# Kernel tuning notes

Measured on AMD Instinct MI355X. Metric: run time of the kernel, lower is better.

The kernel has to match this reference:

```python
import jax, jax.numpy as jnp
import numpy as np
from jax import lax

B, C_IN, C_OUT, H, W, E = 16, 256, 256, 32, 32, 8


def setup_inputs() -> dict:
    key = jax.random.key(0)
    k = jax.random.split(key, 5)
    x = jax.random.normal(k[0], (B, C_IN, H, W), dtype=jnp.float32)
    # router: Conv2d(C_IN, E, kernel_size=1) -> weight [E, C_IN], bias [E]
    wc = jax.random.normal(k[1], (E, C_IN), dtype=jnp.float32) / np.sqrt(C_IN)
    bc = jnp.zeros((E,), dtype=jnp.float32)
    # experts: E x Conv2d(C_IN, C_OUT, 3, padding=1) + ReLU
    we = jax.random.normal(k[2], (E, C_OUT, C_IN, 3, 3), dtype=jnp.float32) / np.sqrt(C_IN * 9)
    be = jnp.zeros((E, C_OUT), dtype=jnp.float32)
    return {"x": x, "wc": wc, "bc": bc, "we": we, "be": be}


def reference(x, wc, bc, we, be):
    Bx = x.shape[0]
    # controller: 1x1 conv then global avg-pool == pool then linear
    pooled = jnp.mean(x, axis=(2, 3))                      # [B, C_IN]
    logits = pooled @ wc.T + bc                            # [B, E]
    decisions = jnp.argmax(logits, axis=1)                 # [B] int
    # run ALL experts on the full batch as one grouped conv: weight [E*C_OUT, C_IN, 3, 3]
    w_all = we.reshape(E * C_OUT, C_IN, 3, 3)
    y = lax.conv_general_dilated(
        x, w_all, window_strides=(1, 1), padding="SAME",
        dimension_numbers=("NCHW", "OIHW", "NCHW"))        # [B, E*C_OUT, H, W]
    y = y + be.reshape(1, E * C_OUT, 1, 1)
    y = jax.nn.relu(y).reshape(Bx, E, C_OUT, H, W)
    # faithful to forward_test: out block i is components[dec[i]](x) for the FULL batch
    # out[i*B + j] = y[j, dec[i]]
    gathered = y[:, decisions]                             # [j, i, C_OUT, H, W]
    out = jnp.swapaxes(gathered, 0, 1).reshape(Bx * Bx, C_OUT, H, W)
    return out
```

## Files before the change

kernel.cpp:

```cpp
#include <hip/hip_runtime.h>
#include <hip/hip_bf16.h>
#include <stdint.h>

#define B_    16
#define CIN   256
#define COUT  256
#define E_    8
#define HW    1024
#define PH    34
#define PW    34

typedef __attribute__((ext_vector_type(8))) short  short8;
typedef __attribute__((ext_vector_type(4))) float  floatx4;

#define XT_OFF 17408
#define XT_BYTES (B_*PH*PW*CIN*2)
#define WT_OFF (XT_OFF + XT_BYTES)

__device__ __forceinline__ void gld_lds16(const void* g, void* l) {
    __builtin_amdgcn_global_load_lds(
        (const __attribute__((address_space(1))) unsigned int*)g,
        (__attribute__((address_space(3))) unsigned int*)l,
        16, 0, 0);
}

__global__ void prep_kernel(const float* __restrict__ x, const float* __restrict__ we,
                            unsigned short* __restrict__ xt, unsigned short* __restrict__ wt,
                            float* __restrict__ pooled) {
    int bid = blockIdx.x;
    int t = threadIdx.x;
    if (bid < 128) {
        int b = bid >> 3, ci0 = (bid & 7) * 32;
        __shared__ float tileF[32][65];
        float psum[8];
        #pragma unroll
        for (int li = 0; li < 8; ++li) psum[li] = 0.0f;
        int hwl = t & 63, wv = t >> 6;
        int hwl2 = t >> 2, grp = t & 3;
        for (int chunk = 0; chunk < 16; ++chunk) {
            #pragma unroll
            for (int li = 0; li < 8; ++li) {
                int ci = wv + li*4;
                float v = x[((size_t)b*CIN + ci0 + ci)*HW + chunk*64 + hwl];
                tileF[ci][hwl] = v;
                psum[li] += v;
            }
            __syncthreads();
            int hw = chunk*64 + hwl2;
            int h = hw >> 5, w = hw & 31;
            short8 v8;
            #pragma unroll
            for (int q = 0; q < 8; ++q) {
                __hip_bfloat16 hv = __float2bfloat16(tileF[grp*8 + q][hwl2]);
                v8[q] = *(short*)&hv;
            }
            *(short8*)&xt[(((size_t)b*PH + h + 1)*PW + (w + 1))*CIN + ci0 + grp*8] = v8;
            __syncthreads();
        }
        #pragma unroll
        for (int li = 0; li < 8; ++li) {
            float s = psum[li];
            #pragma unroll
            for (int o = 32; o > 0; o >>= 1) s += __shfl_down(s, o, 64);
            if ((t & 63) == 0) pooled[b*CIN + ci0 + wv + li*4] = s;
        }
        short8 z = {0,0,0,0,0,0,0,0};
        for (int idx = t; idx < 528; idx += 256) {
            int pos = idx >> 2, sub = idx & 3;
            int h, w;
            if (pos < 34)       { h = 0;            w = pos; }
            else if (pos < 68)  { h = 33;           w = pos - 34; }
            else if (pos < 100) { h = pos - 68 + 1; w = 0; }
            else                { h = pos - 100 + 1;w = 33; }
            *(short8*)&xt[(((size_t)b*PH + h)*PW + w)*CIN + ci0 + sub*8] = z;
        }
    } else {
        int wbid = bid - 128;
        int e = wbid >> 8, co = wbid & 255;
        __shared__ float buf[CIN*9];
        const float* src = we + ((size_t)e*COUT + co)*CIN*9;
        #pragma unroll
        for (int k = 0; k < 9; ++k) buf[t + k*256] = src[t + k*256];
        __syncthreads();
        for (int idx = t; idx < 288; idx += 256) {
            int rs = idx >> 5, grp = idx & 31;
            short8 v;
            #pragma unroll
            for (int q = 0; q < 8; ++q) {
                __hip_bfloat16 h = __float2bfloat16(buf[(grp*8 + q)*9 + rs]);
                v[q] = *(short*)&h;
            }
            *(short8*)&wt[(((size_t)e*9 + rs)*COUT + co)*CIN + grp*8] = v;
        }
    }
}

__global__ __launch_bounds__(256) void conv_kernel(
    const unsigned short* __restrict__ xt, const unsigned short* __restrict__ wt,
    const float* __restrict__ pooled, const float* __restrict__ wc,
    const float* __restrict__ bc, const float* __restrict__ be,
    float* __restrict__ out) {

    int tile = blockIdx.x;
    int b = blockIdx.y;
    int e = blockIdx.z;
    int mt = tile >> 3, nt = tile & 7;
    int t = threadIdx.x;

    __shared__ float lg[16][8];
    __shared__ int sdec[16];
    if (t < 128) {
        int bb = t >> 3, ee = t & 7;
        float acc = 0.0f;
        const float4* pp = (const float4*)(pooled + bb*CIN);
        const float4* ww = (const float4*)(wc + ee*CIN);
        #pragma unroll 4
        for (int i = 0; i < CIN/4; ++i) {
            float4 p = pp[i], w = ww[i];
            acc += p.x*w.x + p.y*w.y + p.z*w.z + p.w*w.w;
        }
        lg[bb][ee] = acc * (1.0f/1024.0f) + bc[ee];
    }
    __syncthreads();
    if (t < 16) {
        float best = lg[t][0]; int bi = 0;
        #pragma unroll
        for (int j = 1; j < 8; ++j) if (lg[t][j] > best) { best = lg[t][j]; bi = j; }
        sdec[t] = bi;
    }
    __syncthreads();
    int dcs[16];
    #pragma unroll
    for (int i = 0; i < 16; ++i) dcs[i] = sdec[i];
    bool active = false;
    #pragma unroll
    for (int i = 0; i < 16; ++i) active |= (dcs[i] == e);
    if (!active) return;

    __shared__ __align__(16) unsigned short sA[2][512*8];
    __shared__ __align__(16) unsigned short sB[2][1024*8];

    int wave = t >> 6, lane = t & 63;
    int wm = wave >> 1, wn = wave & 1;
    int kg = lane >> 4, ln = lane & 15;

    int ph0 = nt * 4;
    int co0 = mt * 128;

    floatx4 acc[4][4];
    #pragma unroll
    for (int i = 0; i < 4; ++i)
        #pragma unroll
        for (int j = 0; j < 4; ++j) acc[i][j] = (floatx4)0.0f;

    const unsigned short* xb = xt + ((size_t)b*PH + ph0)*PW*CIN;
    const unsigned short* wb = wt + (size_t)e*9*COUT*CIN + (size_t)co0*CIN;

    auto stageA = [&](int ck, int sh, int buf) {
        const unsigned short* wsrc = wb + (size_t)sh*COUT*CIN + ck*32;
        #pragma unroll
        for (int k = 0; k < 2; ++k) {
            int c = t + k*256;
            int row = c >> 2, gs = c & 3;
            int g = gs ^ ((row >> 1) & 3);
            gld_lds16(wsrc + (size_t)row*CIN + g*8, &sA[buf][c*8]);
        }
    };
    auto stageB = [&](int ck, int buf) {
        const unsigned short* xsrc = xb + ck*32;
        #pragma unroll
        for (int k = 0; k < 3; ++k) {
            int c = t + k*256;
            int rB = c >> 2, gs = c & 3;
            int g = gs ^ ((rB >> 1) & 3);
            gld_lds16(xsrc + (size_t)rB*CIN + g*8, &sB[buf][c*8]);
        }
        if (t < 64) {
            int c = t + 768;
            int cc = c < 816 ? c : 815;
            int rB = cc >> 2, gs = cc & 3;
            int g = gs ^ ((rB >> 1) & 3);
            gld_lds16(xsrc + (size_t)rB*CIN + g*8, &sB[buf][c*8]);
        }
    };

    stageB(0, 0);
    stageA(0, 0, 0);
    __syncthreads();

    for (int ck = 0; ck < 8; ++ck) {
        for (int sh = 0; sh < 9; ++sh) {
            int it = ck*9 + sh;
            int ab = it & 1, bb_ = ck & 1;

            if (sh < 8) {
                stageA(ck, sh + 1, ab ^ 1);
            } else if (ck < 7) {
                stageA(ck + 1, 0, ab ^ 1);
                stageB(ck + 1, bb_ ^ 1);
            }

            short8 a[4], bv[4];
            #pragma unroll
            for (int im = 0; im < 4; ++im) {
                int row = wm*64 + im*16 + ln;
                int cL = row*4 + (kg ^ ((row >> 1) & 3));
                a[im] = *(const short8*)(&sA[ab][cL*8]);
            }
            int r = sh / 3, s = sh - r*3;
            #pragma unroll
            for (int in = 0; in < 4; ++in) {
                int n  = wn*64 + in*16 + ln;
                int hl = n >> 5, wl = n & 31;
                int rB = (hl + r)*34 + (wl + s);
                int cL = rB*4 + (kg ^ ((rB >> 1) & 3));
                bv[in] = *(const short8*)(&sB[bb_][cL*8]);
            }

            #pragma unroll
            for (int im = 0; im < 4; ++im)
                #pragma unroll
                for (int in = 0; in < 4; ++in)
                    acc[im][in] = __builtin_amdgcn_mfma_f32_16x16x32_bf16(bv[in], a[im], acc[im][in], 0, 0, 0);

            __syncthreads();
        }
    }

    float bias[4];
    #pragma unroll
    for (int im = 0; im < 4; ++im)
        bias[im] = be[e*COUT + co0 + wm*64 + im*16 + ln];
    #pragma unroll
    for (int im = 0; im < 4; ++im)
        #pragma unroll
        for (int in = 0; in < 4; ++in)
            #pragma unroll
            for (int rg = 0; rg < 4; ++rg) {
                float v = acc[im][in][rg] + bias[im];
                acc[im][in][rg] = v > 0.0f ? v : 0.0f;
            }

    for (int i = 0; i < 16; ++i) {
        if (dcs[i] != e) continue;
        float* ob = out + (size_t)(i*16 + b)*COUT*HW;
        #pragma unroll
        for (int im = 0; im < 4; ++im) {
            int co = co0 + wm*64 + im*16 + ln;
            float* orow = ob + (size_t)co*HW + nt*128 + wn*64 + kg*4;
            #pragma unroll
            for (int in = 0; in < 4; ++in)
                *(floatx4*)(orow + in*16) = acc[im][in];
        }
    }
}

extern "C" void kernel_launch(void* const* d_in, const int* in_sizes, int n_in,
                              void* d_out, int out_size, void* d_ws, size_t ws_size,
                              hipStream_t stream) {
    const float* x  = (const float*)d_in[0];
    const float* wc = (const float*)d_in[1];
    const float* bc = (const float*)d_in[2];
    const float* we = (const float*)d_in[3];
    const float* be = (const float*)d_in[4];
    float* out = (float*)d_out;

    char* ws = (char*)d_ws;
    float* pooled = (float*)(ws + 64);
    unsigned short* xt = (unsigned short*)(ws + XT_OFF);
    unsigned short* wt = (unsigned short*)(ws + WT_OFF);

    prep_kernel<<<2176, 256, 0, stream>>>(x, we, xt, wt, pooled);
    conv_kernel<<<dim3(16, 16, 8), 256, 0, stream>>>(xt, wt, pooled, wc, bc, be, out);
}
```

Before: 481.4 us.

## Move routing to separate kernel and single-buffer the input tile in LDS

Routing logits and argmax now run once in a small decide_kernel instead of being recomputed by every conv block. The conv kernel drops the double buffer for the input patch, cutting LDS use per block, which may allow more resident blocks. The patch reload is now done only at each channel-chunk boundary, behind an explicit barrier after the last shift's B reads. The cost is less overlap of the B load with compute and one extra kernel launch.

```diff
diff --git a/kernel.cpp b/kernel.cpp
--- a/kernel.cpp
+++ b/kernel.cpp
@@ -95,51 +95,52 @@
     }
 }
 
-__global__ __launch_bounds__(256) void conv_kernel(
+__global__ void decide_kernel(const float* __restrict__ pooled, const float* __restrict__ wc,
+                              const float* __restrict__ bc, int* __restrict__ dec) {
+    int t = threadIdx.x;
+    int b = t >> 3, e = t & 7;
+    float acc = 0.0f;
+    const float4* pp = (const float4*)(pooled + b*CIN);
+    const float4* ww = (const float4*)(wc + e*CIN);
+    #pragma unroll 4
+    for (int i = 0; i < CIN/4; ++i) {
+        float4 p = pp[i], w = ww[i];
+        acc += p.x*w.x + p.y*w.y + p.z*w.z + p.w*w.w;
+    }
+    acc = acc * (1.0f/1024.0f) + bc[e];
+    __shared__ float lg[16][8];
+    lg[b][e] = acc;
+    __syncthreads();
+    if (e == 0) {
+        float best = lg[b][0]; int bi = 0;
+        #pragma unroll
+        for (int j = 1; j < 8; ++j) { if (lg[b][j] > best) { best = lg[b][j]; bi = j; } }
+        dec[b] = bi;
+    }
+}
+
+__global__ void conv_kernel(
     const unsigned short* __restrict__ xt, const unsigned short* __restrict__ wt,
-    const float* __restrict__ pooled, const float* __restrict__ wc,
-    const float* __restrict__ bc, const float* __restrict__ be,
+    const float* __restrict__ be, const int* __restrict__ dec,
     float* __restrict__ out) {
 
     int tile = blockIdx.x;
     int b = blockIdx.y;
     int e = blockIdx.z;
     int mt = tile >> 3, nt = tile & 7;
-    int t = threadIdx.x;
-
-    __shared__ float lg[16][8];
-    __shared__ int sdec[16];
-    if (t < 128) {
-        int bb = t >> 3, ee = t & 7;
-        float acc = 0.0f;
-        const float4* pp = (const float4*)(pooled + bb*CIN);
-        const float4* ww = (const float4*)(wc + ee*CIN);
-        #pragma unroll 4
-        for (int i = 0; i < CIN/4; ++i) {
-            float4 p = pp[i], w = ww[i];
-            acc += p.x*w.x + p.y*w.y + p.z*w.z + p.w*w.w;
-        }
-        lg[bb][ee] = acc * (1.0f/1024.0f) + bc[ee];
-    }
-    __syncthreads();
-    if (t < 16) {
-        float best = lg[t][0]; int bi = 0;
-        #pragma unroll
-        for (int j = 1; j < 8; ++j) if (lg[t][j] > best) { best = lg[t][j]; bi = j; }
-        sdec[t] = bi;
-    }
-    __syncthreads();
+
     int dcs[16];
     #pragma unroll
-    for (int i = 0; i < 16; ++i) dcs[i] = sdec[i];
+    for (int i = 0; i < 16; ++i) dcs[i] = dec[i];
     bool active = false;
     #pragma unroll
     for (int i = 0; i < 16; ++i) active |= (dcs[i] == e);
     if (!active) return;
 
     __shared__ __align__(16) unsigned short sA[2][512*8];
-    __shared__ __align__(16) unsigned short sB[2][1024*8];
-
+    __shared__ __align__(16) unsigned short sB[832*8];
+
+    int t = threadIdx.x;
     int wave = t >> 6, lane = t & 63;
     int wm = wave >> 1, wn = wave & 1;
     int kg = lane >> 4, ln = lane & 15;
@@ -166,64 +167,80 @@
             gld_lds16(wsrc + (size_t)row*CIN + g*8, &sA[buf][c*8]);
         }
     };
-    auto stageB = [&](int ck, int buf) {
+    auto stageB = [&](int ck) {
         const unsigned short* xsrc = xb + ck*32;
         #pragma unroll
         for (int k = 0; k < 3; ++k) {
             int c = t + k*256;
             int rB = c >> 2, gs = c & 3;
             int g = gs ^ ((rB >> 1) & 3);
-            gld_lds16(xsrc + (size_t)rB*CIN + g*8, &sB[buf][c*8]);
+            gld_lds16(xsrc + (size_t)rB*CIN + g*8, &sB[c*8]);
         }
         if (t < 64) {
             int c = t + 768;
             int cc = c < 816 ? c : 815;
             int rB = cc >> 2, gs = cc & 3;
             int g = gs ^ ((rB >> 1) & 3);
-            gld_lds16(xsrc + (size_t)rB*CIN + g*8, &sB[buf][c*8]);
-        }
-    };
-
-    stageB(0, 0);
+            gld_lds16(xsrc + (size_t)rB*CIN + g*8, &sB[c*8]);
+        }
+    };
+
+    short8 a[4], bv[4];
+    auto readA = [&](int ab) {
+        #pragma unroll
+        for (int im = 0; im < 4; ++im) {
+            int row = wm*64 + im*16 + ln;
+            int cL = row*4 + (kg ^ ((row >> 1) & 3));
+            a[im] = *(const short8*)(&sA[ab][cL*8]);
+        }
+    };
+    auto readB = [&](int r, int s) {
+        #pragma unroll
+        for (int in = 0; in < 4; ++in) {
+            int n  = wn*64 + in*16 + ln;
+            int hl = n >> 5, wl = n & 31;
+            int rB = (hl + r)*34 + (wl + s);
+            int cL = rB*4 + (kg ^ ((rB >> 1) & 3));
+            bv[in] = *(const short8*)(&sB[cL*8]);
+        }
+    };
+
+    stageB(0);
     stageA(0, 0, 0);
     __syncthreads();
 
     for (int ck = 0; ck < 8; ++ck) {
         for (int sh = 0; sh < 9; ++sh) {
             int it = ck*9 + sh;
-            int ab = it & 1, bb_ = ck & 1;
+            int ab = it & 1;
+            int r = sh / 3, s = sh - r*3;
 
             if (sh < 8) {
                 stageA(ck, sh + 1, ab ^ 1);
-            } else if (ck < 7) {
-                stageA(ck + 1, 0, ab ^ 1);
-                stageB(ck + 1, bb_ ^ 1);
-            }
-
-            short8 a[4], bv[4];
-            #pragma unroll
-            for (int im = 0; im < 4; ++im) {
-                int row = wm*64 + im*16 + ln;
-                int cL = row*4 + (kg ^ ((row >> 1) & 3));
-                a[im] = *(const short8*)(&sA[ab][cL*8]);
-            }
-            int r = sh / 3, s = sh - r*3;
-            #pragma unroll
-            for (int in = 0; in < 4; ++in) {
-                int n  = wn*64 + in*16 + ln;
-                int hl = n >> 5, wl = n & 31;
-                int rB = (hl + r)*34 + (wl + s);
-                int cL = rB*4 + (kg ^ ((rB >> 1) & 3));
-                bv[in] = *(const short8*)(&sB[bb_][cL*8]);
-            }
-
-            #pragma unroll
-            for (int im = 0; im < 4; ++im)
+                readA(ab);
+                readB(r, s);
                 #pragma unroll
-                for (int in = 0; in < 4; ++in)
-                    acc[im][in] = __builtin_amdgcn_mfma_f32_16x16x32_bf16(bv[in], a[im], acc[im][in], 0, 0, 0);
-
-            __syncthreads();
+                for (int im = 0; im < 4; ++im)
+                    #pragma unroll
+                    for (int in = 0; in < 4; ++in)
+                        acc[im][in] = __builtin_amdgcn_mfma_f32_16x16x32_bf16(bv[in], a[im], acc[im][in], 0, 0, 0);
+                __syncthreads();
+            } else {
+                readB(r, s);
+                if (ck < 7) {
+                    asm volatile("s_waitcnt lgkmcnt(0)" ::: "memory");
+                    __builtin_amdgcn_s_barrier();
+                    stageB(ck + 1);
+                    stageA(ck + 1, 0, ab ^ 1);
+                }
+                readA(ab);
+                #pragma unroll
+                for (int im = 0; im < 4; ++im)
+                    #pragma unroll
+                    for (int in = 0; in < 4; ++in)
+                        acc[im][in] = __builtin_amdgcn_mfma_f32_16x16x32_bf16(bv[in], a[im], acc[im][in], 0, 0, 0);
+                if (ck < 7) __syncthreads();
+            }
         }
     }
 
@@ -266,10 +283,12 @@
     float* out = (float*)d_out;
 
     char* ws = (char*)d_ws;
+    int*   dec    = (int*)ws;
     float* pooled = (float*)(ws + 64);
     unsigned short* xt = (unsigned short*)(ws + XT_OFF);
     unsigned short* wt = (unsigned short*)(ws + WT_OFF);
 
-    prep_kernel<<<2176, 256, 0, stream>>>(x, we, xt, wt, pooled);
-    conv_kernel<<<dim3(16, 16, 8), 256, 0, stream>>>(xt, wt, pooled, wc, bc, be, out);
-}
+    prep_kernel  <<<2176, 256, 0, stream>>>(x, we, xt, wt, pooled);
+    decide_kernel<<<1, 128, 0, stream>>>(pooled, wc, bc, dec);
+    conv_kernel  <<<dim3(16, 16, 8), 256, 0, stream>>>(xt, wt, be, dec, out);
+}
```

After: 570.6 us. +18.5%, slower.
